# Kernel optimization log

Hardware: AMD Instinct MI355X
Metric: run time of the kernel (lower is better)

## Reference

```python
import jax, jax.numpy as jnp
import numpy as np

ETA = 1.0
BETA = 0.6
LN_EPS = 1e-5


def layer_norm(x, scale, bias):
    mu = x.mean(-1, keepdims=True)
    var = ((x - mu) ** 2).mean(-1, keepdims=True)
    return (x - mu) / jnp.sqrt(var + LN_EPS) * scale + bias


def setup_inputs() -> dict:
    B, N, S, C, D = 8, 2048, 16, 32, 128
    key = jax.random.key(0)
    ks = jax.random.split(key, 10)
    X_short = jax.random.normal(ks[0], (B, N, S, C), dtype=jnp.float32)
    # binary temporal validity mask (float, as multiplied in the original)
    mask_short = (jax.random.uniform(ks[1], (B, N, S)) > 0.3).astype(jnp.float32)
    A_stat = jax.random.uniform(ks[2], (N, N), dtype=jnp.float32)
    M_mask = jax.random.randint(ks[3], (N, N), 0, 2).astype(jnp.int32)
    M_mask = M_mask.at[jnp.arange(N), jnp.arange(N)].set(1)  # keep self-edges so no all-masked row
    node_reliab = jax.random.uniform(ks[4], (B, N), dtype=jnp.float32)
    # learned parameters (stored (in, out) so application is x @ W)
    W_proj = jax.random.normal(ks[5], (C, D), dtype=jnp.float32) / np.sqrt(C)
    Wq = jax.random.normal(ks[6], (D, D), dtype=jnp.float32) / np.sqrt(D)
    Wk = jax.random.normal(ks[7], (D, D), dtype=jnp.float32) / np.sqrt(D)
    W_lin = jax.random.normal(ks[8], (D, D), dtype=jnp.float32) / np.sqrt(D)
    ln1_scale = jnp.ones((D,), jnp.float32)
    ln1_bias = jnp.zeros((D,), jnp.float32)
    ln2_scale = jnp.ones((D,), jnp.float32)
    ln2_bias = jnp.zeros((D,), jnp.float32)
    return {
        "X_short": X_short, "mask_short": mask_short, "A_stat": A_stat,
        "M_mask": M_mask, "node_reliab": node_reliab,
        "W_proj": W_proj, "Wq": Wq, "Wk": Wk, "W_lin": W_lin,
        "ln1_scale": ln1_scale, "ln1_bias": ln1_bias,
        "ln2_scale": ln2_scale, "ln2_bias": ln2_bias,
    }


def reference(X_short, mask_short, A_stat, M_mask, node_reliab,
              W_proj, Wq, Wk, W_lin, ln1_scale, ln1_bias, ln2_scale, ln2_bias):
    D = W_proj.shape[1]
    # masked temporal mean pooling over S
    denom = jnp.maximum(mask_short.sum(axis=2, keepdims=True), 1.0)      # (B,N,1)
    x = (X_short * mask_short[..., None]).sum(axis=2) / denom            # (B,N,C)
    Hn = x @ W_proj                                                      # (B,N,D)
    # dynamic graph attention
    Q = Hn @ Wq
    K = Hn @ Wk
    logits = jnp.einsum('bnd,bmd->bnm', Q, K) / jnp.sqrt(jnp.float32(D))
    p = jnp.clip(A_stat, 1e-3, 1.0 - 1e-3)
    bias = jnp.log(p / (1.0 - p))                                        # logit
    logits = logits + ETA * bias[None]
    edge = (M_mask != 0)[None]                                           # (1,N,N)
    logits = jnp.where(edge, logits, -jnp.inf)
    Adyn = jax.nn.softmax(logits, axis=-1)                               # (B,N,N)
    # fuse with static adjacency, reliability scaling, mask, row-renormalize
    A_fuse = BETA * Adyn + (1.0 - BETA) * A_stat[None]
    r = jnp.clip(node_reliab, 0.0, 1.0)                                  # (B,N)
    A_fuse = A_fuse * r[:, :, None] * r[:, None, :]
    A_fuse = A_fuse * M_mask.astype(A_fuse.dtype)[None]
    A_fuse = A_fuse / (A_fuse.sum(axis=-1, keepdims=True) + 1e-8)
    # propagate: A @ H -> linear -> relu -> (dropout=eval identity) -> LN -> outer LN
    H = jnp.einsum('bnm,bmd->bnd', A_fuse, Hn)
    H = H @ W_lin
    H = layer_norm(jax.nn.relu(H), ln1_scale, ln1_bias)
    out = layer_norm(H, ln2_scale, ln2_bias)
    return out, A_fuse
```

## Files before the change

kernel.cpp:

```cpp
#include <hip/hip_runtime.h>
#include <math.h>

#define BB 8
#define NN 2048
#define SS 16
#define CC 32
#define DD 128

typedef unsigned short u16;
typedef __attribute__((ext_vector_type(8))) short bf16x8;
typedef __attribute__((ext_vector_type(4))) float f32x4;

__device__ inline u16 f2bf(float f) {
    union { float f; unsigned u; } c; c.f = f;
    unsigned r = c.u + 0x7fff + ((c.u >> 16) & 1);
    return (u16)(r >> 16);
}
__device__ inline float bf2f(u16 h) {
    union { unsigned u; float f; } c; c.u = ((unsigned)h) << 16;
    return c.f;
}
__device__ inline u16 f2h(float f) {
    union { _Float16 h; u16 u; } c; c.h = (_Float16)f;
    return c.u;
}
__device__ inline float h2f(u16 u) {
    union { _Float16 h; u16 v; } c; c.v = u;
    return (float)c.h;
}
__device__ inline float clamp01(float v) { return fminf(fmaxf(v, 0.f), 1.f); }

__global__ __launch_bounds__(256) void prep_kernel(const float* __restrict__ Astat,
                                                   const int* __restrict__ Mm,
                                                   const float* __restrict__ Wproj,
                                                   const float* __restrict__ Wq,
                                                   const float* __restrict__ Wk,
                                                   const float* __restrict__ Wl,
                                                   unsigned* __restrict__ lam,
                                                   float* __restrict__ Wpq,
                                                   float* __restrict__ Wpk,
                                                   u16* __restrict__ WlT) {
    int bx = blockIdx.x;
    if (bx < 4096) {
        size_t g = ((size_t)bx * 256 + threadIdx.x) * 4;
        float4 a4 = *(const float4*)&Astat[g];
        int4 m4 = *(const int4*)&Mm[g];
        float a[4] = {a4.x, a4.y, a4.z, a4.w};
        int mm[4] = {m4.x, m4.y, m4.z, m4.w};
        unsigned pw[4];
#pragma unroll
        for (int j = 0; j < 4; ++j) {
            float p = fminf(fmaxf(a[j], 1e-3f), 1.f - 1e-3f);
            float l = __logf(p / (1.f - p));
            u16 lg = mm[j] ? f2h(l) : (u16)0xFC00;
            u16 ab = mm[j] ? f2bf(a[j]) : (u16)0;
            pw[j] = ((unsigned)ab << 16) | lg;
        }
        *(uint4*)&lam[g] = make_uint4(pw[0], pw[1], pw[2], pw[3]);
    } else if (bx < 4128) {
        int i = (bx - 4096) * 256 + threadIdx.x;
        int d = i & 127;
        int c = (i >> 7) & 31;
        int mat = i >> 12;
        const float* Wt = mat ? Wk : Wq;
        float acc = 0.f;
#pragma unroll 4
        for (int e = 0; e < DD; ++e)
            acc = fmaf(Wproj[c * DD + e], Wt[e * DD + d], acc);
        (mat ? Wpk : Wpq)[c * DD + d] = acc;
    } else {
        int i = (bx - 4128) * 256 + threadIdx.x;
        int dp = i >> 7, d = i & 127;
        WlT[dp * DD + d] = f2bf(Wl[d * DD + dp]);
    }
}

__global__ __launch_bounds__(256) void proj3_kernel(const float* __restrict__ X,
                                                    const float* __restrict__ Msk,
                                                    const float* __restrict__ Wproj,
                                                    const float* __restrict__ Wpq,
                                                    const float* __restrict__ Wpk,
                                                    u16* __restrict__ HnT,
                                                    u16* __restrict__ Qb,
                                                    u16* __restrict__ Kb) {
    __shared__ float wp[CC * DD], wq[CC * DD], wk[CC * DD];
    __shared__ float xs[CC * 36];
    int t = threadIdx.x;
    for (int i = t; i < CC * DD; i += 256) {
        wp[i] = Wproj[i];
        wq[i] = Wpq[i];
        wk[i] = Wpk[i];
    }
    int rbase = blockIdx.x * 32;
    {
        int row = t >> 3, cg = t & 7;
        const float* xrow = X + ((size_t)(rbase + row) * SS) * CC + cg * 4;
        const float* mrow = Msk + (size_t)(rbase + row) * SS;
        float4 acc = make_float4(0.f, 0.f, 0.f, 0.f);
        float msum = 0.f;
#pragma unroll
        for (int s = 0; s < SS; ++s) {
            float mv = mrow[s];
            float4 xv = *(const float4*)&xrow[s * CC];
            msum += mv;
            acc.x = fmaf(xv.x, mv, acc.x);
            acc.y = fmaf(xv.y, mv, acc.y);
            acc.z = fmaf(xv.z, mv, acc.z);
            acc.w = fmaf(xv.w, mv, acc.w);
        }
        float inv = 1.f / fmaxf(msum, 1.0f);
        xs[(cg * 4 + 0) * 36 + row] = acc.x * inv;
        xs[(cg * 4 + 1) * 36 + row] = acc.y * inv;
        xs[(cg * 4 + 2) * 36 + row] = acc.z * inv;
        xs[(cg * 4 + 3) * 36 + row] = acc.w * inv;
    }
    __syncthreads();

    int col = t & 127;
    int g = t >> 7;
    float ah[16], aq[16], ak[16];
#pragma unroll
    for (int i = 0; i < 16; ++i) { ah[i] = 0.f; aq[i] = 0.f; ak[i] = 0.f; }

#pragma unroll 4
    for (int k = 0; k < CC; ++k) {
        float wpv = wp[k * DD + col], wqv = wq[k * DD + col], wkv = wk[k * DD + col];
        const float4* xp = (const float4*)&xs[k * 36 + g * 16];
        float4 a0 = xp[0], a1 = xp[1], a2 = xp[2], a3 = xp[3];
        float xv[16] = {a0.x, a0.y, a0.z, a0.w, a1.x, a1.y, a1.z, a1.w,
                        a2.x, a2.y, a2.z, a2.w, a3.x, a3.y, a3.z, a3.w};
#pragma unroll
        for (int i = 0; i < 16; ++i) {
            ah[i] = fmaf(xv[i], wpv, ah[i]);
            aq[i] = fmaf(xv[i], wqv, aq[i]);
            ak[i] = fmaf(xv[i], wkv, ak[i]);
        }
    }
    const float scale = 0.08838834764831845f;
#pragma unroll
    for (int i = 0; i < 16; ++i) {
        size_t row = (size_t)(rbase + g * 16 + i);
        Qb[row * DD + col] = f2bf(aq[i] * scale);
        Kb[row * DD + col] = f2bf(ak[i]);
    }
    int b = rbase >> 11;
    int n0 = (rbase & (NN - 1)) + g * 16;
    u16* hp = HnT + (size_t)b * DD * NN + (size_t)col * NN + n0;
    unsigned pk[8];
#pragma unroll
    for (int i = 0; i < 8; ++i)
        pk[i] = (unsigned)f2bf(ah[2 * i]) | ((unsigned)f2bf(ah[2 * i + 1]) << 16);
    *(uint4*)&hp[0] = make_uint4(pk[0], pk[1], pk[2], pk[3]);
    *(uint4*)&hp[8] = make_uint4(pk[4], pk[5], pk[6], pk[7]);
}

#define LQT 136
#define LPT 72
#define LWT 136
__global__ __launch_bounds__(512) void prop_kernel(
        const u16* __restrict__ Qb, const u16* __restrict__ Kb,
        const unsigned* __restrict__ lam,
        const float* __restrict__ rel,
        const u16* __restrict__ HnT, const u16* __restrict__ WlT,
        const float* __restrict__ s1, const float* __restrict__ b1,
        const float* __restrict__ s2, const float* __restrict__ b2,
        float* __restrict__ Af, float* __restrict__ out) {
    __shared__ union {
        struct { u16 Qs[32 * LQT]; u16 Ks[64 * LQT];
                 u16 Bs[128 * LPT]; u16 As[32 * LPT]; } ck;
        struct { u16 Ws[128 * LWT]; u16 Hs[32 * LWT]; } fin;
    } sm;
    __shared__ float redS[128], redQ[128], redA[128];
    __shared__ float2 MV[32];
    __shared__ float2 cfs[32];
    int rt = blockIdx.x, b = blockIdx.y;
    int R0 = rt * 32;
    int t = threadIdx.x;
    int lane = t & 63, w = t >> 6, q = lane >> 4, r16 = lane & 15;
    int i2 = w >> 2, j2 = w & 3;
    int wr = i2 * 16;
    int wc = j2 * 32;

    const u16* Qg = Qb + ((size_t)b * NN + R0) * DD;
    {
        int row = t >> 4, seg = t & 15;
        *(uint4*)&sm.ck.Qs[row * LQT + seg * 8] = *(const uint4*)&Qg[row * DD + seg * 8];
    }

    const u16* Kg = Kb + (size_t)b * NN * DD;
    const u16* Bg = HnT + (size_t)b * DD * NN;
    int krow0 = t >> 4, krow1 = 32 + (t >> 4), kseg = (t & 15) * 8;
    int bd0 = t >> 3, bd1 = 64 + (t >> 3), bsg = (t & 7) * 8;
    int mloc = j2 * 16 + r16;
    int n0 = R0 + wr + q * 4;
    const size_t lb0 = (size_t)n0 * NN + mloc;

    float ER0 = 0.f, ER1 = 0.f, ER2 = 0.f, ER3 = 0.f;
    float LR0 = 0.f, LR1 = 0.f, LR2 = 0.f, LR3 = 0.f;
    float LA0 = 0.f, LA1 = 0.f, LA2 = 0.f, LA3 = 0.f;

    uint4 pk0 = *(const uint4*)&Kg[(size_t)krow0 * DD + kseg];
    uint4 pk1 = *(const uint4*)&Kg[(size_t)krow1 * DD + kseg];
    unsigned pl0 = lam[lb0];
    unsigned pl1 = lam[lb0 + NN];
    unsigned pl2 = lam[lb0 + 2 * NN];
    unsigned pl3 = lam[lb0 + 3 * NN];

    for (int kc = 0; kc < NN; kc += 64) {
        __syncthreads();
        *(uint4*)&sm.ck.Ks[krow0 * LQT + kseg] = pk0;
        *(uint4*)&sm.ck.Ks[krow1 * LQT + kseg] = pk1;
        if (kc + 64 < NN) {
            int kn = kc + 64;
            pk0 = *(const uint4*)&Kg[(size_t)(kn + krow0) * DD + kseg];
            pk1 = *(const uint4*)&Kg[(size_t)(kn + krow1) * DD + kseg];
        }
        __syncthreads();
        f32x4 sa = (f32x4){0.f, 0.f, 0.f, 0.f};
#pragma unroll
        for (int ksp = 0; ksp < 4; ++ksp) {
            int ko = ksp * 32 + q * 8;
            bf16x8 a0 = *(const bf16x8*)&sm.ck.Qs[(wr + r16) * LQT + ko];
            bf16x8 b0 = *(const bf16x8*)&sm.ck.Ks[(j2 * 16 + r16) * LQT + ko];
            sa = __builtin_amdgcn_mfma_f32_16x16x32_bf16(a0, b0, sa, 0, 0, 0);
        }
        int mb = kc + mloc;
        float rm = clamp01(rel[b * NN + mb]);
        float e0 = __expf(sa[0] + h2f((u16)(pl0 & 0xffff)));
        float a0v = bf2f((u16)(pl0 >> 16));
        float e1 = __expf(sa[1] + h2f((u16)(pl1 & 0xffff)));
        float a1v = bf2f((u16)(pl1 >> 16));
        float e2 = __expf(sa[2] + h2f((u16)(pl2 & 0xffff)));
        float a2v = bf2f((u16)(pl2 >> 16));
        float e3 = __expf(sa[3] + h2f((u16)(pl3 & 0xffff)));
        float a3v = bf2f((u16)(pl3 >> 16));
        ER0 += e0; ER1 += e1; ER2 += e2; ER3 += e3;
        LR0 = fmaf(e0, rm, LR0); LR1 = fmaf(e1, rm, LR1);
        LR2 = fmaf(e2, rm, LR2); LR3 = fmaf(e3, rm, LR3);
        LA0 = fmaf(a0v, rm, LA0); LA1 = fmaf(a1v, rm, LA1);
        LA2 = fmaf(a2v, rm, LA2); LA3 = fmaf(a3v, rm, LA3);
        if (kc + 64 < NN) {
            size_t lb = lb0 + (kc + 64);
            pl0 = lam[lb];
            pl1 = lam[lb + NN];
            pl2 = lam[lb + 2 * NN];
            pl3 = lam[lb + 3 * NN];
        }
    }
    pk0 = *(const uint4*)&Kg[(size_t)krow0 * DD + kseg];
    pk1 = *(const uint4*)&Kg[(size_t)krow1 * DD + kseg];
    uint4 pb0 = *(const uint4*)&Bg[(size_t)bd0 * NN + bsg];
    uint4 pb1 = *(const uint4*)&Bg[(size_t)bd1 * NN + bsg];
    pl0 = lam[lb0];
    pl1 = lam[lb0 + NN];
    pl2 = lam[lb0 + 2 * NN];
    pl3 = lam[lb0 + 3 * NN];

#pragma unroll
    for (int off = 1; off < 16; off <<= 1) {
        ER0 += __shfl_xor(ER0, off); ER1 += __shfl_xor(ER1, off);
        ER2 += __shfl_xor(ER2, off); ER3 += __shfl_xor(ER3, off);
        LR0 += __shfl_xor(LR0, off); LR1 += __shfl_xor(LR1, off);
        LR2 += __shfl_xor(LR2, off); LR3 += __shfl_xor(LR3, off);
        LA0 += __shfl_xor(LA0, off); LA1 += __shfl_xor(LA1, off);
        LA2 += __shfl_xor(LA2, off); LA3 += __shfl_xor(LA3, off);
    }
    if (r16 == 0) {
        int row = wr + q * 4;
        redS[j2 * 32 + row + 0] = ER0; redQ[j2 * 32 + row + 0] = LR0; redA[j2 * 32 + row + 0] = LA0;
        redS[j2 * 32 + row + 1] = ER1; redQ[j2 * 32 + row + 1] = LR1; redA[j2 * 32 + row + 1] = LA1;
        redS[j2 * 32 + row + 2] = ER2; redQ[j2 * 32 + row + 2] = LR2; redA[j2 * 32 + row + 2] = LA2;
        redS[j2 * 32 + row + 3] = ER3; redQ[j2 * 32 + row + 3] = LR3; redA[j2 * 32 + row + 3] = LA3;
    }
    __syncthreads();
    if (t < 32) {
        float es = redS[t] + redS[32 + t] + redS[64 + t] + redS[96 + t];
        float lr = redQ[t] + redQ[32 + t] + redQ[64 + t] + redQ[96 + t];
        float la = redA[t] + redA[32 + t] + redA[64 + t] + redA[96 + t];
        float rn = clamp01(rel[b * NN + R0 + t]);
        float inv = 1.f / es;
        float fsum = rn * (0.6f * lr * inv + 0.4f * la);
        float nrm = 1.f / (fsum + 1e-8f);
        cfs[t] = make_float2(0.6f * inv * rn * nrm, 0.4f * rn * nrm);
    }

    f32x4 acc[2];
    acc[0] = (f32x4){0.f, 0.f, 0.f, 0.f};
    acc[1] = (f32x4){0.f, 0.f, 0.f, 0.f};

    for (int kc = 0; kc < NN; kc += 64) {
        __syncthreads();
        *(uint4*)&sm.ck.Ks[krow0 * LQT + kseg] = pk0;
        *(uint4*)&sm.ck.Ks[krow1 * LQT + kseg] = pk1;
        *(uint4*)&sm.ck.Bs[bd0 * LPT + bsg] = pb0;
        *(uint4*)&sm.ck.Bs[bd1 * LPT + bsg] = pb1;
        if (kc + 64 < NN) {
            int kn = kc + 64;
            pk0 = *(const uint4*)&Kg[(size_t)(kn + krow0) * DD + kseg];
            pk1 = *(const uint4*)&Kg[(size_t)(kn + krow1) * DD + kseg];
            pb0 = *(const uint4*)&Bg[(size_t)bd0 * NN + kn + bsg];
            pb1 = *(const uint4*)&Bg[(size_t)bd1 * NN + kn + bsg];
        }
        __syncthreads();
        f32x4 sa = (f32x4){0.f, 0.f, 0.f, 0.f};
#pragma unroll
        for (int ksp = 0; ksp < 4; ++ksp) {
            int ko = ksp * 32 + q * 8;
            bf16x8 a0 = *(const bf16x8*)&sm.ck.Qs[(wr + r16) * LQT + ko];
            bf16x8 b0 = *(const bf16x8*)&sm.ck.Ks[(j2 * 16 + r16) * LQT + ko];
            sa = __builtin_amdgcn_mfma_f32_16x16x32_bf16(a0, b0, sa, 0, 0, 0);
        }
        int mb = kc + mloc;
        float rm = clamp01(rel[b * NN + mb]);
        float2 cf0 = cfs[wr + q * 4 + 0];
        float2 cf1 = cfs[wr + q * 4 + 1];
        float2 cf2 = cfs[wr + q * 4 + 2];
        float2 cf3 = cfs[wr + q * 4 + 3];
        float e0 = __expf(sa[0] + h2f((u16)(pl0 & 0xffff)));
        float v0 = rm * fmaf(e0, cf0.x, bf2f((u16)(pl0 >> 16)) * cf0.y);
        float e1 = __expf(sa[1] + h2f((u16)(pl1 & 0xffff)));
        float v1 = rm * fmaf(e1, cf1.x, bf2f((u16)(pl1 >> 16)) * cf1.y);
        float e2 = __expf(sa[2] + h2f((u16)(pl2 & 0xffff)));
        float v2 = rm * fmaf(e2, cf2.x, bf2f((u16)(pl2 >> 16)) * cf2.y);
        float e3 = __expf(sa[3] + h2f((u16)(pl3 & 0xffff)));
        float v3 = rm * fmaf(e3, cf3.x, bf2f((u16)(pl3 >> 16)) * cf3.y);
        size_t ob = ((size_t)b * NN + n0) * NN + mb;
        Af[ob] = v0;
        Af[ob + NN] = v1;
        Af[ob + 2 * NN] = v2;
        Af[ob + 3 * NN] = v3;
        sm.ck.As[(wr + q * 4 + 0) * LPT + mloc] = f2bf(v0);
        sm.ck.As[(wr + q * 4 + 1) * LPT + mloc] = f2bf(v1);
        sm.ck.As[(wr + q * 4 + 2) * LPT + mloc] = f2bf(v2);
        sm.ck.As[(wr + q * 4 + 3) * LPT + mloc] = f2bf(v3);
        if (kc + 64 < NN) {
            size_t lb = lb0 + (kc + 64);
            pl0 = lam[lb];
            pl1 = lam[lb + NN];
            pl2 = lam[lb + 2 * NN];
            pl3 = lam[lb + 3 * NN];
        }
        __syncthreads();
#pragma unroll
        for (int kst = 0; kst < 2; ++kst) {
            int ko = kst * 32 + q * 8;
            bf16x8 a0 = *(const bf16x8*)&sm.ck.As[(wr + r16) * LPT + ko];
            bf16x8 b0 = *(const bf16x8*)&sm.ck.Bs[(wc + r16) * LPT + ko];
            bf16x8 b1v = *(const bf16x8*)&sm.ck.Bs[(wc + 16 + r16) * LPT + ko];
            acc[0] = __builtin_amdgcn_mfma_f32_16x16x32_bf16(a0, b0, acc[0], 0, 0, 0);
            acc[1] = __builtin_amdgcn_mfma_f32_16x16x32_bf16(a0, b1v, acc[1], 0, 0, 0);
        }
    }

    __syncthreads();
#pragma unroll
    for (int rep = 0; rep < 4; ++rep) {
        int e = rep * 512 + t;
        int dp = e >> 4, seg = e & 15;
        *(uint4*)&sm.fin.Ws[dp * LWT + seg * 8] = *(const uint4*)&WlT[dp * DD + seg * 8];
    }
#pragma unroll
    for (int j = 0; j < 2; ++j)
#pragma unroll
        for (int r = 0; r < 4; ++r)
            sm.fin.Hs[(wr + q * 4 + r) * LWT + wc + j * 16 + r16] = f2bf(acc[j][r]);
    __syncthreads();

    f32x4 c2[2];
    c2[0] = (f32x4){0.f, 0.f, 0.f, 0.f};
    c2[1] = (f32x4){0.f, 0.f, 0.f, 0.f};
#pragma unroll
    for (int ksp = 0; ksp < 4; ++ksp) {
        int ko = ksp * 32 + q * 8;
        bf16x8 a0 = *(const bf16x8*)&sm.fin.Hs[(wr + r16) * LWT + ko];
        bf16x8 b0 = *(const bf16x8*)&sm.fin.Ws[(wc + r16) * LWT + ko];
        bf16x8 b1v = *(const bf16x8*)&sm.fin.Ws[(wc + 16 + r16) * LWT + ko];
        c2[0] = __builtin_amdgcn_mfma_f32_16x16x32_bf16(a0, b0, c2[0], 0, 0, 0);
        c2[1] = __builtin_amdgcn_mfma_f32_16x16x32_bf16(a0, b1v, c2[1], 0, 0, 0);
    }
    float v[2][4];
#pragma unroll
    for (int j = 0; j < 2; ++j)
#pragma unroll
        for (int r = 0; r < 4; ++r)
            v[j][r] = fmaxf(c2[j][r], 0.f);

    int c0 = wc + r16, c1 = wc + 16 + r16;
    float s1c0 = s1[c0], s1c1 = s1[c1], b1c0 = b1[c0], b1c1 = b1[c1];
    float s2c0 = s2[c0], s2c1 = s2[c1], b2c0 = b2[c0], b2c1 = b2[c1];
    int g4 = (w & 3) * 32;

#pragma unroll
    for (int r = 0; r < 4; ++r) {
        float s = v[0][r] + v[1][r];
        float qq = v[0][r] * v[0][r] + v[1][r] * v[1][r];
#pragma unroll
        for (int off = 1; off < 16; off <<= 1) {
            s += __shfl_xor(s, off);
            qq += __shfl_xor(qq, off);
        }
        if (r16 == 0) {
            int row = wr + q * 4 + r;
            redS[g4 + row] = s;
            redQ[g4 + row] = qq;
        }
    }
    __syncthreads();
    if (t < 32) {
        float s = redS[t] + redS[32 + t] + redS[64 + t] + redS[96 + t];
        float qq = redQ[t] + redQ[32 + t] + redQ[64 + t] + redQ[96 + t];
        float mu = s * (1.f / 128.f);
        float var = qq * (1.f / 128.f) - mu * mu;
        MV[t] = make_float2(mu, 1.f / sqrtf(var + 1e-5f));
    }
    __syncthreads();
    float y[2][4];
#pragma unroll
    for (int r = 0; r < 4; ++r) {
        float2 mv = MV[wr + q * 4 + r];
        y[0][r] = (v[0][r] - mv.x) * mv.y * s1c0 + b1c0;
        y[1][r] = (v[1][r] - mv.x) * mv.y * s1c1 + b1c1;
    }
    __syncthreads();
#pragma unroll
    for (int r = 0; r < 4; ++r) {
        float s = y[0][r] + y[1][r];
        float qq = y[0][r] * y[0][r] + y[1][r] * y[1][r];
#pragma unroll
        for (int off = 1; off < 16; off <<= 1) {
            s += __shfl_xor(s, off);
            qq += __shfl_xor(qq, off);
        }
        if (r16 == 0) {
            int row = wr + q * 4 + r;
            redS[g4 + row] = s;
            redQ[g4 + row] = qq;
        }
    }
    __syncthreads();
    if (t < 32) {
        float s = redS[t] + redS[32 + t] + redS[64 + t] + redS[96 + t];
        float qq = redQ[t] + redQ[32 + t] + redQ[64 + t] + redQ[96 + t];
        float mu = s * (1.f / 128.f);
        float var = qq * (1.f / 128.f) - mu * mu;
        MV[t] = make_float2(mu, 1.f / sqrtf(var + 1e-5f));
    }
    __syncthreads();
#pragma unroll
    for (int r = 0; r < 4; ++r) {
        float2 mv = MV[wr + q * 4 + r];
        size_t o = ((size_t)b * NN + R0 + wr + q * 4 + r) * DD;
        out[o + c0] = (y[0][r] - mv.x) * mv.y * s2c0 + b2c0;
        out[o + c1] = (y[1][r] - mv.x) * mv.y * s2c1 + b2c1;
    }
}

extern "C" void kernel_launch(void* const* d_in, const int* in_sizes, int n_in,
                              void* d_out, int out_size, void* d_ws, size_t ws_size,
                              hipStream_t stream) {
    const float* X = (const float*)d_in[0];
    const float* Msk = (const float*)d_in[1];
    const float* Astat = (const float*)d_in[2];
    const int* Mm = (const int*)d_in[3];
    const float* rel = (const float*)d_in[4];
    const float* Wproj = (const float*)d_in[5];
    const float* Wq = (const float*)d_in[6];
    const float* Wk = (const float*)d_in[7];
    const float* Wlin = (const float*)d_in[8];
    const float* s1 = (const float*)d_in[9];
    const float* b1 = (const float*)d_in[10];
    const float* s2 = (const float*)d_in[11];
    const float* b2 = (const float*)d_in[12];

    float* outMain = (float*)d_out;
    float* Afuse = outMain + (size_t)BB * NN * DD;

    float* w_ = (float*)d_ws;
    float* Wpq = w_;
    float* Wpk = w_ + 4096;
    u16* WlT = (u16*)(w_ + 8192);
    u16* Qb = (u16*)(w_ + 16384);
    u16* Kb = (u16*)(w_ + 1064960);
    u16* HnT = (u16*)(w_ + 2113536);
    unsigned* lam = (unsigned*)(w_ + 3162112);

    prep_kernel<<<dim3(4192), dim3(256), 0, stream>>>(
        Astat, Mm, Wproj, Wq, Wk, Wlin, lam, Wpq, Wpk, WlT);
    proj3_kernel<<<dim3(512), dim3(256), 0, stream>>>(X, Msk, Wproj, Wpq, Wpk, HnT, Qb, Kb);

    prop_kernel<<<dim3(64, 8), dim3(512), 0, stream>>>(
        Qb, Kb, lam, rel, HnT, WlT, s1, b1, s2, b2, Afuse, outMain);
}
```

Before: 307.4 us.

## Double-buffer K and Hn tiles in LDS and keep Q fragments in registers

Both passes over the key dimension now use ping-pong LDS buffers for the K and Hn^T tiles. Each iteration writes the next tile while computing on the current one, which removes one barrier per iteration. Global loads are prefetched two chunks ahead into registers. The Q tile is held as four bf16x8 register fragments per lane instead of being reread from LDS every iteration. The cost is a larger LDS footprint, which could lower the number of resident blocks per CU, and more register pressure.

```diff
diff --git a/kernel.cpp b/kernel.cpp
--- a/kernel.cpp
+++ b/kernel.cpp
@@ -166,8 +166,8 @@
         const float* __restrict__ s2, const float* __restrict__ b2,
         float* __restrict__ Af, float* __restrict__ out) {
     __shared__ union {
-        struct { u16 Qs[32 * LQT]; u16 Ks[64 * LQT];
-                 u16 Bs[128 * LPT]; u16 As[32 * LPT]; } ck;
+        struct { u16 Ks[2][64 * LQT]; u16 Bs[2][128 * LPT];
+                 u16 As[32 * LPT]; } ck;
         struct { u16 Ws[128 * LWT]; u16 Hs[32 * LWT]; } fin;
     } sm;
     __shared__ float redS[128], redQ[128], redA[128];
@@ -181,12 +181,6 @@
     int wr = i2 * 16;
     int wc = j2 * 32;
 
-    const u16* Qg = Qb + ((size_t)b * NN + R0) * DD;
-    {
-        int row = t >> 4, seg = t & 15;
-        *(uint4*)&sm.ck.Qs[row * LQT + seg * 8] = *(const uint4*)&Qg[row * DD + seg * 8];
-    }
-
     const u16* Kg = Kb + (size_t)b * NN * DD;
     const u16* Bg = HnT + (size_t)b * DD * NN;
     int krow0 = t >> 4, krow1 = 32 + (t >> 4), kseg = (t & 15) * 8;
@@ -195,36 +189,54 @@
     int n0 = R0 + wr + q * 4;
     const size_t lb0 = (size_t)n0 * NN + mloc;
 
+    const u16* qrow = Qb + ((size_t)b * NN + R0 + wr + r16) * DD;
+    bf16x8 qf0 = *(const bf16x8*)&qrow[q * 8];
+    bf16x8 qf1 = *(const bf16x8*)&qrow[32 + q * 8];
+    bf16x8 qf2 = *(const bf16x8*)&qrow[64 + q * 8];
+    bf16x8 qf3 = *(const bf16x8*)&qrow[96 + q * 8];
+
     float ER0 = 0.f, ER1 = 0.f, ER2 = 0.f, ER3 = 0.f;
     float LR0 = 0.f, LR1 = 0.f, LR2 = 0.f, LR3 = 0.f;
     float LA0 = 0.f, LA1 = 0.f, LA2 = 0.f, LA3 = 0.f;
 
-    uint4 pk0 = *(const uint4*)&Kg[(size_t)krow0 * DD + kseg];
-    uint4 pk1 = *(const uint4*)&Kg[(size_t)krow1 * DD + kseg];
+    uint4 rk0 = *(const uint4*)&Kg[(size_t)krow0 * DD + kseg];
+    uint4 rk1 = *(const uint4*)&Kg[(size_t)krow1 * DD + kseg];
+    *(uint4*)&sm.ck.Ks[0][krow0 * LQT + kseg] = rk0;
+    *(uint4*)&sm.ck.Ks[0][krow1 * LQT + kseg] = rk1;
+    rk0 = *(const uint4*)&Kg[(size_t)(64 + krow0) * DD + kseg];
+    rk1 = *(const uint4*)&Kg[(size_t)(64 + krow1) * DD + kseg];
     unsigned pl0 = lam[lb0];
     unsigned pl1 = lam[lb0 + NN];
     unsigned pl2 = lam[lb0 + 2 * NN];
     unsigned pl3 = lam[lb0 + 3 * NN];
-
-    for (int kc = 0; kc < NN; kc += 64) {
-        __syncthreads();
-        *(uint4*)&sm.ck.Ks[krow0 * LQT + kseg] = pk0;
-        *(uint4*)&sm.ck.Ks[krow1 * LQT + kseg] = pk1;
-        if (kc + 64 < NN) {
-            int kn = kc + 64;
-            pk0 = *(const uint4*)&Kg[(size_t)(kn + krow0) * DD + kseg];
-            pk1 = *(const uint4*)&Kg[(size_t)(kn + krow1) * DD + kseg];
-        }
-        __syncthreads();
+    __syncthreads();
+
+    for (int ic = 0; ic < 32; ++ic) {
+        const int p = ic & 1;
+        const u16* Kc = sm.ck.Ks[p];
+        u16* Kn = sm.ck.Ks[p ^ 1];
+        if (ic + 1 < 32) {
+            *(uint4*)&Kn[krow0 * LQT + kseg] = rk0;
+            *(uint4*)&Kn[krow1 * LQT + kseg] = rk1;
+        }
+        if (ic + 2 < 32) {
+            int kn2 = (ic + 2) * 64;
+            rk0 = *(const uint4*)&Kg[(size_t)(kn2 + krow0) * DD + kseg];
+            rk1 = *(const uint4*)&Kg[(size_t)(kn2 + krow1) * DD + kseg];
+        }
         f32x4 sa = (f32x4){0.f, 0.f, 0.f, 0.f};
-#pragma unroll
-        for (int ksp = 0; ksp < 4; ++ksp) {
-            int ko = ksp * 32 + q * 8;
-            bf16x8 a0 = *(const bf16x8*)&sm.ck.Qs[(wr + r16) * LQT + ko];
-            bf16x8 b0 = *(const bf16x8*)&sm.ck.Ks[(j2 * 16 + r16) * LQT + ko];
-            sa = __builtin_amdgcn_mfma_f32_16x16x32_bf16(a0, b0, sa, 0, 0, 0);
-        }
-        int mb = kc + mloc;
+        {
+            const u16* kr = &Kc[(j2 * 16 + r16) * LQT + q * 8];
+            bf16x8 b0 = *(const bf16x8*)&kr[0];
+            sa = __builtin_amdgcn_mfma_f32_16x16x32_bf16(qf0, b0, sa, 0, 0, 0);
+            b0 = *(const bf16x8*)&kr[32];
+            sa = __builtin_amdgcn_mfma_f32_16x16x32_bf16(qf1, b0, sa, 0, 0, 0);
+            b0 = *(const bf16x8*)&kr[64];
+            sa = __builtin_amdgcn_mfma_f32_16x16x32_bf16(qf2, b0, sa, 0, 0, 0);
+            b0 = *(const bf16x8*)&kr[96];
+            sa = __builtin_amdgcn_mfma_f32_16x16x32_bf16(qf3, b0, sa, 0, 0, 0);
+        }
+        int mb = ic * 64 + mloc;
         float rm = clamp01(rel[b * NN + mb]);
         float e0 = __expf(sa[0] + h2f((u16)(pl0 & 0xffff)));
         float a0v = bf2f((u16)(pl0 >> 16));
@@ -239,18 +251,20 @@
         LR2 = fmaf(e2, rm, LR2); LR3 = fmaf(e3, rm, LR3);
         LA0 = fmaf(a0v, rm, LA0); LA1 = fmaf(a1v, rm, LA1);
         LA2 = fmaf(a2v, rm, LA2); LA3 = fmaf(a3v, rm, LA3);
-        if (kc + 64 < NN) {
-            size_t lb = lb0 + (kc + 64);
+        if (ic + 1 < 32) {
+            size_t lb = lb0 + (ic + 1) * 64;
             pl0 = lam[lb];
             pl1 = lam[lb + NN];
             pl2 = lam[lb + 2 * NN];
             pl3 = lam[lb + 3 * NN];
         }
-    }
-    pk0 = *(const uint4*)&Kg[(size_t)krow0 * DD + kseg];
-    pk1 = *(const uint4*)&Kg[(size_t)krow1 * DD + kseg];
-    uint4 pb0 = *(const uint4*)&Bg[(size_t)bd0 * NN + bsg];
-    uint4 pb1 = *(const uint4*)&Bg[(size_t)bd1 * NN + bsg];
+        __syncthreads();
+    }
+
+    rk0 = *(const uint4*)&Kg[(size_t)krow0 * DD + kseg];
+    rk1 = *(const uint4*)&Kg[(size_t)krow1 * DD + kseg];
+    uint4 rb0 = *(const uint4*)&Bg[(size_t)bd0 * NN + bsg];
+    uint4 rb1 = *(const uint4*)&Bg[(size_t)bd1 * NN + bsg];
     pl0 = lam[lb0];
     pl1 = lam[lb0 + NN];
     pl2 = lam[lb0 + 2 * NN];
@@ -283,34 +297,52 @@
         float nrm = 1.f / (fsum + 1e-8f);
         cfs[t] = make_float2(0.6f * inv * rn * nrm, 0.4f * rn * nrm);
     }
+    *(uint4*)&sm.ck.Ks[0][krow0 * LQT + kseg] = rk0;
+    *(uint4*)&sm.ck.Ks[0][krow1 * LQT + kseg] = rk1;
+    *(uint4*)&sm.ck.Bs[0][bd0 * LPT + bsg] = rb0;
+    *(uint4*)&sm.ck.Bs[0][bd1 * LPT + bsg] = rb1;
+    rk0 = *(const uint4*)&Kg[(size_t)(64 + krow0) * DD + kseg];
+    rk1 = *(const uint4*)&Kg[(size_t)(64 + krow1) * DD + kseg];
+    rb0 = *(const uint4*)&Bg[(size_t)bd0 * NN + 64 + bsg];
+    rb1 = *(const uint4*)&Bg[(size_t)bd1 * NN + 64 + bsg];
+    __syncthreads();
 
     f32x4 acc[2];
     acc[0] = (f32x4){0.f, 0.f, 0.f, 0.f};
     acc[1] = (f32x4){0.f, 0.f, 0.f, 0.f};
 
-    for (int kc = 0; kc < NN; kc += 64) {
-        __syncthreads();
-        *(uint4*)&sm.ck.Ks[krow0 * LQT + kseg] = pk0;
-        *(uint4*)&sm.ck.Ks[krow1 * LQT + kseg] = pk1;
-        *(uint4*)&sm.ck.Bs[bd0 * LPT + bsg] = pb0;
-        *(uint4*)&sm.ck.Bs[bd1 * LPT + bsg] = pb1;
-        if (kc + 64 < NN) {
-            int kn = kc + 64;
-            pk0 = *(const uint4*)&Kg[(size_t)(kn + krow0) * DD + kseg];
-            pk1 = *(const uint4*)&Kg[(size_t)(kn + krow1) * DD + kseg];
-            pb0 = *(const uint4*)&Bg[(size_t)bd0 * NN + kn + bsg];
-            pb1 = *(const uint4*)&Bg[(size_t)bd1 * NN + kn + bsg];
-        }
-        __syncthreads();
+    for (int ic = 0; ic < 32; ++ic) {
+        const int p = ic & 1;
+        const u16* Kc = sm.ck.Ks[p];
+        u16* Kn = sm.ck.Ks[p ^ 1];
+        const u16* Bc = sm.ck.Bs[p];
+        u16* Bn = sm.ck.Bs[p ^ 1];
+        if (ic + 1 < 32) {
+            *(uint4*)&Kn[krow0 * LQT + kseg] = rk0;
+            *(uint4*)&Kn[krow1 * LQT + kseg] = rk1;
+            *(uint4*)&Bn[bd0 * LPT + bsg] = rb0;
+            *(uint4*)&Bn[bd1 * LPT + bsg] = rb1;
+        }
+        if (ic + 2 < 32) {
+            int kn2 = (ic + 2) * 64;
+            rk0 = *(const uint4*)&Kg[(size_t)(kn2 + krow0) * DD + kseg];
+            rk1 = *(const uint4*)&Kg[(size_t)(kn2 + krow1) * DD + kseg];
+            rb0 = *(const uint4*)&Bg[(size_t)bd0 * NN + kn2 + bsg];
+            rb1 = *(const uint4*)&Bg[(size_t)bd1 * NN + kn2 + bsg];
+        }
         f32x4 sa = (f32x4){0.f, 0.f, 0.f, 0.f};
-#pragma unroll
-        for (int ksp = 0; ksp < 4; ++ksp) {
-            int ko = ksp * 32 + q * 8;
-            bf16x8 a0 = *(const bf16x8*)&sm.ck.Qs[(wr + r16) * LQT + ko];
-            bf16x8 b0 = *(const bf16x8*)&sm.ck.Ks[(j2 * 16 + r16) * LQT + ko];
-            sa = __builtin_amdgcn_mfma_f32_16x16x32_bf16(a0, b0, sa, 0, 0, 0);
-        }
-        int mb = kc + mloc;
+        {
+            const u16* kr = &Kc[(j2 * 16 + r16) * LQT + q * 8];
+            bf16x8 b0 = *(const bf16x8*)&kr[0];
+            sa = __builtin_amdgcn_mfma_f32_16x16x32_bf16(qf0, b0, sa, 0, 0, 0);
+            b0 = *(const bf16x8*)&kr[32];
+            sa = __builtin_amdgcn_mfma_f32_16x16x32_bf16(qf1, b0, sa, 0, 0, 0);
+            b0 = *(const bf16x8*)&kr[64];
+            sa = __builtin_amdgcn_mfma_f32_16x16x32_bf16(qf2, b0, sa, 0, 0, 0);
+            b0 = *(const bf16x8*)&kr[96];
+            sa = __builtin_amdgcn_mfma_f32_16x16x32_bf16(qf3, b0, sa, 0, 0, 0);
+        }
+        int mb = ic * 64 + mloc;
         float rm = clamp01(rel[b * NN + mb]);
         float2 cf0 = cfs[wr + q * 4 + 0];
         float2 cf1 = cfs[wr + q * 4 + 1];
@@ -333,8 +365,8 @@
         sm.ck.As[(wr + q * 4 + 1) * LPT + mloc] = f2bf(v1);
         sm.ck.As[(wr + q * 4 + 2) * LPT + mloc] = f2bf(v2);
         sm.ck.As[(wr + q * 4 + 3) * LPT + mloc] = f2bf(v3);
-        if (kc + 64 < NN) {
-            size_t lb = lb0 + (kc + 64);
+        if (ic + 1 < 32) {
+            size_t lb = lb0 + (ic + 1) * 64;
             pl0 = lam[lb];
             pl1 = lam[lb + NN];
             pl2 = lam[lb + 2 * NN];
@@ -345,14 +377,14 @@
         for (int kst = 0; kst < 2; ++kst) {
             int ko = kst * 32 + q * 8;
             bf16x8 a0 = *(const bf16x8*)&sm.ck.As[(wr + r16) * LPT + ko];
-            bf16x8 b0 = *(const bf16x8*)&sm.ck.Bs[(wc + r16) * LPT + ko];
-            bf16x8 b1v = *(const bf16x8*)&sm.ck.Bs[(wc + 16 + r16) * LPT + ko];
+            bf16x8 b0 = *(const bf16x8*)&Bc[(wc + r16) * LPT + ko];
+            bf16x8 b1v = *(const bf16x8*)&Bc[(wc + 16 + r16) * LPT + ko];
             acc[0] = __builtin_amdgcn_mfma_f32_16x16x32_bf16(a0, b0, acc[0], 0, 0, 0);
             acc[1] = __builtin_amdgcn_mfma_f32_16x16x32_bf16(a0, b1v, acc[1], 0, 0, 0);
         }
-    }
-
-    __syncthreads();
+        __syncthreads();
+    }
+
 #pragma unroll
     for (int rep = 0; rep < 4; ++rep) {
         int e = rep * 512 + t;
```

Result: faster. 296.6 us, median of 2 (-3.5%).
